# Performance work log

Measured on AMD Instinct MI355X. Metric: run time of the kernel, lower is better.

Reference implementation:

```python
import jax, jax.numpy as jnp
import numpy as np

NH = 32          # num_attention_heads
LAYER_ID = 3     # -> query_key_layer_scaling_coeff = 4.0
ROPE_BASE = 10000.0


def setup_inputs() -> dict:
    key = jax.random.key(0)
    k1, k2, k3, k4, k5 = jax.random.split(key, 5)
    S, B, H = 2048, 1, 4096
    hidden_states = jax.random.normal(k1, (S, B, H), dtype=jnp.float32)
    position_ids = jnp.broadcast_to(jnp.arange(S, dtype=jnp.int64)[None, :], (B, S))
    # causal mask: True means masked out (torch masked_fill semantics)
    mask = jnp.triu(jnp.ones((S, S), dtype=bool), k=1)[None, None, :, :]
    qkv_w = jax.random.normal(k2, (3 * H, H), dtype=jnp.float32) * 0.02
    qkv_b = jax.random.normal(k3, (3 * H,), dtype=jnp.float32) * 0.02
    dense_w = jax.random.normal(k4, (H, H), dtype=jnp.float32) * 0.02
    dense_b = jax.random.normal(k5, (H,), dtype=jnp.float32) * 0.02
    return {"hidden_states": hidden_states, "position_ids": position_ids, "mask": mask,
            "qkv_w": qkv_w, "qkv_b": qkv_b, "dense_w": dense_w, "dense_b": dense_b}


def _rotate_half(x):
    h = x.shape[-1] // 2
    return jnp.concatenate((-x[..., h:], x[..., :h]), axis=-1)


def reference(hidden_states, position_ids, mask, qkv_w, qkv_b, dense_w, dense_b):
    S, B, H = hidden_states.shape
    nh = NH
    hd = H // nh
    coeff = float(LAYER_ID + 1)

    # fused QKV projection: [S, B, 3H] -> [S, B, nh, 3*hd] -> split
    mixed = hidden_states @ qkv_w.T + qkv_b
    mixed = mixed.reshape(S, B, nh, 3 * hd)
    q, k, v = jnp.split(mixed, 3, axis=-1)  # each [S, B, nh, hd]

    # rotary embedding indexed by position_ids (transposed to [S, B])
    pos = position_ids.T  # [S, B]
    inv_freq = 1.0 / (ROPE_BASE ** (jnp.arange(0, hd, 2, dtype=jnp.float32) / hd))
    freqs = pos.astype(jnp.float32)[..., None] * inv_freq  # [S, B, hd/2]
    emb = jnp.concatenate((freqs, freqs), axis=-1)          # [S, B, hd]
    cos = jnp.cos(emb)[:, :, None, :]                       # [S, B, 1, hd]
    sin = jnp.sin(emb)[:, :, None, :]
    q = q * cos + _rotate_half(q) * sin
    k = k * cos + _rotate_half(k) * sin

    # scaled attention scores with per-layer coefficient
    q = q / (jnp.sqrt(jnp.float32(hd)) * coeff)
    scores = jnp.einsum('sbnh,tbnh->bnst', q, k)            # [B, nh, S, S]
    scores = jnp.where(mask, jnp.float32(-10000.0), scores)
    probs = jax.nn.softmax(scores.astype(jnp.float32) * coeff, axis=-1)
    probs = probs.astype(scores.dtype)

    context = jnp.einsum('bnst,tbnh->sbnh', probs, v).reshape(S, B, H)
    output = context @ dense_w.T + dense_b                  # [S, B, H]
    return output
```

## Files before the change

kernel.cpp:

```cpp
#include <hip/hip_runtime.h>
#include <hip/hip_bf16.h>
#include <cstdint>

#define SQ   2048
#define HIDD 4096
#define NH_  32
#define HD_  128

typedef __attribute__((ext_vector_type(8))) __bf16 bf16x8;
typedef __attribute__((ext_vector_type(4))) float  f32x4;

__device__ __forceinline__ unsigned short f2bf(float f) {
  union { float f; unsigned u; } v; v.f = f;
  return (unsigned short)((v.u + 0x7FFFu + ((v.u >> 16) & 1u)) >> 16);
}
__device__ __forceinline__ float bf2f(unsigned short u) {
  union { unsigned u; float f; } v; v.u = ((unsigned)u) << 16; return v.f;
}
__device__ __forceinline__ void gload16(const void* g, void* l) {
  __builtin_amdgcn_global_load_lds((const __attribute__((address_space(1))) void*)g,
                                   (__attribute__((address_space(3))) void*)l, 16, 0, 0);
}
#define BAR()   asm volatile("s_barrier" ::: "memory")
#define VMC(N)  asm volatile("s_waitcnt vmcnt(" #N ")" ::: "memory")

__global__ __launch_bounds__(256) void k_conv(const float* __restrict__ src,
                                              unsigned short* __restrict__ dst, int n4) {
  int i = blockIdx.x * blockDim.x + threadIdx.x;
  int stride = gridDim.x * blockDim.x;
  for (; i < n4; i += stride) {
    float4 f = ((const float4*)src)[i];
    ushort4 o;
    o.x = f2bf(f.x); o.y = f2bf(f.y); o.z = f2bf(f.z); o.w = f2bf(f.w);
    ((ushort4*)dst)[i] = o;
  }
}

template<int MODE>
__global__ __launch_bounds__(256, 3)
void k_gemm4(const unsigned short* __restrict__ A, const unsigned short* __restrict__ B,
             const float* __restrict__ bias, float* __restrict__ outf,
             unsigned short* __restrict__ qb, unsigned short* __restrict__ kb,
             unsigned short* __restrict__ vb, int K) {
  __shared__ __align__(16) char lds[2 * 24576];
  const int t = threadIdx.x;
  const int lane = t & 63, wc = t >> 6;
  const int lr = lane & 15, lg = lane >> 4;
  const int gx = gridDim.x;
  const int nwg = gx * gridDim.y;
  const int id = blockIdx.y * gx + blockIdx.x;
  const int cpx = nwg >> 3;
  const int swz = (id & 7) * cpx + (id >> 3);
  const int bm = swz % gx, bn = swz / gx;

  const unsigned short* src[6];
  int dst[6];
#pragma unroll
  for (int j = 0; j < 6; ++j) {
    int o = j * 4096 + t * 16;
    dst[j] = o;
    if (o < 8192) {
      int row = o >> 6, colb = o & 63;
      src[j] = A + (size_t)(bm * 128 + row) * K + ((colb ^ ((row & 3) << 4)) >> 1);
    } else {
      int o2 = o - 8192;
      int row = o2 >> 6, colb = o2 & 63;
      src[j] = B + (size_t)(bn * 256 + row) * K + ((colb ^ ((row & 3) << 4)) >> 1);
    }
  }

  f32x4 acc[8][4] = {};
  const int nk = K >> 5;
  const int swF = (lr & 3) << 4;

#pragma unroll
  for (int j = 0; j < 6; ++j) gload16(src[j], lds + dst[j]);

  int c = 0;
  for (int kt = 0; kt < nk; ++kt) {
    char* const bufc = lds + c * 24576;
    char* const bufn = lds + (c ^ 1) * 24576;
    if (kt + 1 < nk) {
      const int koff = (kt + 1) * 32;
#pragma unroll
      for (int j = 0; j < 6; ++j) gload16(src[j] + koff, bufn + dst[j]);
      VMC(6);
    } else {
      VMC(0);
    }
    BAR();

    bf16x8 bfr[4];
#pragma unroll
    for (int n = 0; n < 4; ++n) {
      int row = wc * 64 + n * 16 + lr;
      bfr[n] = *(const bf16x8*)(bufc + 8192 + row * 64 + ((lg * 16) ^ swF));
    }
    __builtin_amdgcn_s_setprio(1);
#pragma unroll
    for (int m = 0; m < 8; ++m) {
      bf16x8 a0 = *(const bf16x8*)(bufc + (m * 16 + lr) * 64 + ((lg * 16) ^ swF));
#pragma unroll
      for (int n = 0; n < 4; ++n)
        acc[m][n] = __builtin_amdgcn_mfma_f32_16x16x32_bf16(a0, bfr[n], acc[m][n], 0, 0, 0);
    }
    __builtin_amdgcn_s_setprio(0);
    BAR();
    c ^= 1;
  }

#pragma unroll
  for (int m = 0; m < 8; ++m) {
    int row0 = bm * 128 + m * 16 + lg * 4;
#pragma unroll
    for (int n = 0; n < 4; ++n) {
      int col = bn * 256 + wc * 64 + n * 16 + lr;
      float bv = bias[col];
      if (MODE == 0) {
        int h = col / 384, rem = col - h * 384;
        int sel = rem >> 7, d = rem & 127;
        unsigned short* dstp = sel == 0 ? qb : (sel == 1 ? kb : vb);
#pragma unroll
        for (int r = 0; r < 4; ++r)
          dstp[((size_t)h * SQ + row0 + r) * HD_ + d] = f2bf(acc[m][n][r] + bv);
      } else {
#pragma unroll
        for (int r = 0; r < 4; ++r)
          outf[(size_t)(row0 + r) * HIDD + col] = acc[m][n][r] + bv;
      }
    }
  }
}

template<int MODE, int BN_>
__global__ __launch_bounds__(256, 2)
void k_gemm3(const unsigned short* __restrict__ A, const unsigned short* __restrict__ B,
             const float* __restrict__ bias, float* __restrict__ outf,
             unsigned short* __restrict__ qb, unsigned short* __restrict__ kb,
             unsigned short* __restrict__ vb, int K) {
  constexpr int NS   = 4 + BN_ / 32;
  constexpr int NF   = BN_ / 64;
  constexpr int BUFB = 16384 + BN_ * 128;
  __shared__ __align__(16) char lds[2 * BUFB];
  const int t = threadIdx.x;
  const int lane = t & 63, wc = t >> 6;
  const int lr = lane & 15, lg = lane >> 4;
  const int gx = gridDim.x;
  const int nwg = gx * gridDim.y;
  const int id = blockIdx.y * gx + blockIdx.x;
  const int cpx = nwg >> 3;
  const int swz = (id & 7) * cpx + (id >> 3);
  const int bm = swz % gx, bn = swz / gx;

  const unsigned short* src[NS];
  int dst[NS];
#pragma unroll
  for (int j = 0; j < NS; ++j) {
    int o = j * 4096 + t * 16;
    dst[j] = o;
    if (o < 16384) {
      int row = o >> 7, colb = o & 127;
      src[j] = A + (size_t)(bm * 128 + row) * K + ((colb ^ ((row & 7) << 4)) >> 1);
    } else {
      int o2 = o - 16384;
      int row = o2 >> 7, colb = o2 & 127;
      src[j] = B + (size_t)(bn * BN_ + row) * K + ((colb ^ ((row & 7) << 4)) >> 1);
    }
  }

  f32x4 acc[8][NF] = {};
  const int nk = K >> 6;
  const int swA = (lr & 7) << 4;

#pragma unroll
  for (int j = 0; j < NS; ++j) gload16(src[j], lds + dst[j]);

  int c = 0;
  for (int kt = 0; kt < nk; ++kt) {
    char* const bufc = lds + c * BUFB;
    char* const bufn = lds + (c ^ 1) * BUFB;
    if (kt + 1 < nk) {
      const int koff = (kt + 1) * 64;
#pragma unroll
      for (int j = 0; j < NS; ++j) gload16(src[j] + koff, bufn + dst[j]);
      if constexpr (NS == 10) VMC(10); else VMC(8);
    } else {
      VMC(0);
    }
    BAR();

    bf16x8 bfr[NF][2];
#pragma unroll
    for (int n = 0; n < NF; ++n) {
      const char* base = bufc + 16384 + (wc * (BN_ / 4) + n * 16 + lr) * 128;
#pragma unroll
      for (int kk = 0; kk < 2; ++kk)
        bfr[n][kk] = *(const bf16x8*)(base + ((kk * 64 + lg * 16) ^ swA));
    }
    __builtin_amdgcn_s_setprio(1);
#pragma unroll
    for (int m = 0; m < 8; ++m) {
      const char* abase = bufc + (m * 16 + lr) * 128;
      bf16x8 a0 = *(const bf16x8*)(abase + ((lg * 16) ^ swA));
      bf16x8 a1 = *(const bf16x8*)(abase + ((64 + lg * 16) ^ swA));
#pragma unroll
      for (int n = 0; n < NF; ++n) {
        acc[m][n] = __builtin_amdgcn_mfma_f32_16x16x32_bf16(a0, bfr[n][0], acc[m][n], 0, 0, 0);
        acc[m][n] = __builtin_amdgcn_mfma_f32_16x16x32_bf16(a1, bfr[n][1], acc[m][n], 0, 0, 0);
      }
    }
    __builtin_amdgcn_s_setprio(0);
    BAR();
    c ^= 1;
  }

#pragma unroll
  for (int m = 0; m < 8; ++m) {
    int row0 = bm * 128 + m * 16 + lg * 4;
#pragma unroll
    for (int n = 0; n < NF; ++n) {
      int col = bn * BN_ + wc * (BN_ / 4) + n * 16 + lr;
      float bv = bias[col];
      if (MODE == 0) {
        int h = col / 384, rem = col - h * 384;
        int sel = rem >> 7, d = rem & 127;
        unsigned short* dstp = sel == 0 ? qb : (sel == 1 ? kb : vb);
#pragma unroll
        for (int r = 0; r < 4; ++r)
          dstp[((size_t)h * SQ + row0 + r) * HD_ + d] = f2bf(acc[m][n][r] + bv);
      } else {
#pragma unroll
        for (int r = 0; r < 4; ++r)
          outf[(size_t)(row0 + r) * HIDD + col] = acc[m][n][r] + bv;
      }
    }
  }
}

__global__ __launch_bounds__(256) void k_rope(unsigned short* __restrict__ q,
                                              unsigned short* __restrict__ k) {
  int idx = blockIdx.x * blockDim.x + threadIdx.x;
  int i = idx & 63;
  int s = (idx >> 6) & (SQ - 1);
  int h = idx >> 17;
  float inv = __expf(-(float)i * (9.210340371976184f / 64.0f));
  float f = (float)s * inv;
  float sn, cs;
  sincosf(f, &sn, &cs);
  size_t base = ((size_t)h * SQ + s) * HD_ + i;
  const float qs = 0.08838834764831845f;
  float q0 = bf2f(q[base]), q1 = bf2f(q[base + 64]);
  q[base]      = f2bf((q0 * cs - q1 * sn) * qs);
  q[base + 64] = f2bf((q1 * cs + q0 * sn) * qs);
  float k0 = bf2f(k[base]), k1 = bf2f(k[base + 64]);
  k[base]      = f2bf(k0 * cs - k1 * sn);
  k[base + 64] = f2bf(k1 * cs + k0 * sn);
}

__global__ __launch_bounds__(256) void k_trans(const unsigned short* __restrict__ v,
                                               unsigned short* __restrict__ vt) {
  __shared__ unsigned short tile[32][33];
  const int h = blockIdx.z;
  const int sb = blockIdx.x * 32, db = blockIdx.y * 32;
  const unsigned short* src = v + (size_t)h * SQ * HD_;
  unsigned short* dst = vt + (size_t)h * HD_ * SQ;
  for (int r = threadIdx.y; r < 32; r += 8)
    tile[r][threadIdx.x] = src[(size_t)(sb + r) * HD_ + db + threadIdx.x];
  __syncthreads();
  for (int r = threadIdx.y; r < 32; r += 8)
    dst[(size_t)(db + r) * SQ + sb + threadIdx.x] = tile[threadIdx.x][r];
}

__global__ __launch_bounds__(256)
void k_attn(const unsigned short* __restrict__ q, const unsigned short* __restrict__ k,
            const unsigned short* __restrict__ vt, unsigned short* __restrict__ ctx) {
  __shared__ __align__(16) unsigned short Ks[64 * 128];
  __shared__ __align__(16) unsigned short Vs[128 * 64];
  __shared__ __align__(16) unsigned short Ps[4][16 * 64];

  const int h = blockIdx.y;
  const int t = threadIdx.x;
  const int lane = t & 63, wv = t >> 6;
  const int lr = lane & 15, lg = lane >> 4;

  const unsigned short* Kg = k + (size_t)h * SQ * HD_;
  const unsigned short* Vg = vt + (size_t)h * HD_ * SQ;
  char* const kl = (char*)Ks;
  char* const vl = (char*)Vs;
  char* const pb = (char*)(Ps[wv]);

  for (int ph = 0; ph < 2; ++ph) {
    const int tph = (ph == 0) ? (int)blockIdx.x : 31 - (int)blockIdx.x;
    const int q0p = tph * 64;
    const int qrow = wv * 16 + lg * 4;

    const unsigned short* Q = q + ((size_t)h * SQ + q0p + wv * 16) * HD_;
    bf16x8 qf[4];
#pragma unroll
    for (int kk = 0; kk < 4; ++kk)
      qf[kk] = *(const bf16x8*)(Q + (size_t)lr * HD_ + kk * 32 + lg * 8);

    f32x4 ot[8] = {};
    float m_r[4], l_r[4];
#pragma unroll
    for (int r = 0; r < 4; ++r) { m_r[r] = -1e30f; l_r[r] = 0.f; }

    const int nkt = tph + 1;
    for (int kt = 0; kt < nkt; ++kt) {
      const int kv0 = kt * 64;
      __syncthreads();
#pragma unroll
      for (int it = 0; it < 4; ++it) {
        int o = it * 4096 + t * 16;
        int krow = o >> 8, kcb = o & 255;
        int kscb = kcb ^ ((krow & 7) << 4);
        gload16(Kg + (size_t)(kv0 + krow) * HD_ + (kscb >> 1), kl + o);
        int vrow = o >> 7, vcb = o & 127;
        int vscb = vcb ^ ((vrow & 7) << 4);
        gload16(Vg + (size_t)vrow * SQ + kv0 + (vscb >> 1), vl + o);
      }
      __syncthreads();

      f32x4 sc[4] = {};
#pragma unroll
      for (int ct = 0; ct < 4; ++ct) {
        int row = ct * 16 + lr;
        const char* kbase = kl + row * 256;
#pragma unroll
        for (int kk = 0; kk < 4; ++kk) {
          bf16x8 kf = *(const bf16x8*)(kbase + ((kk * 64 + lg * 16) ^ ((row & 7) << 4)));
          sc[ct] = __builtin_amdgcn_mfma_f32_16x16x32_bf16(qf[kk], kf, sc[ct], 0, 0, 0);
        }
      }

      if (kt == tph) {
#pragma unroll
        for (int ct = 0; ct < 4; ++ct) {
          int col = ct * 16 + lr;
#pragma unroll
          for (int r = 0; r < 4; ++r)
            if (col > qrow + r) sc[ct][r] = -1e30f;
        }
      }

      float tmax[4];
#pragma unroll
      for (int r = 0; r < 4; ++r)
        tmax[r] = fmaxf(fmaxf(sc[0][r], sc[1][r]), fmaxf(sc[2][r], sc[3][r]));
#pragma unroll
      for (int off = 1; off < 16; off <<= 1)
#pragma unroll
        for (int r = 0; r < 4; ++r) tmax[r] = fmaxf(tmax[r], __shfl_xor(tmax[r], off, 64));

      float scf[4];
#pragma unroll
      for (int r = 0; r < 4; ++r) {
        float mn = fmaxf(m_r[r], tmax[r]);
        scf[r] = __expf(m_r[r] - mn);
        m_r[r] = mn;
      }
      float pr[4][4], rsum[4];
#pragma unroll
      for (int r = 0; r < 4; ++r) rsum[r] = 0.f;
#pragma unroll
      for (int ct = 0; ct < 4; ++ct)
#pragma unroll
        for (int r = 0; r < 4; ++r) {
          pr[ct][r] = __expf(sc[ct][r] - m_r[r]);
          rsum[r] += pr[ct][r];
        }
#pragma unroll
      for (int off = 1; off < 16; off <<= 1)
#pragma unroll
        for (int r = 0; r < 4; ++r) rsum[r] += __shfl_xor(rsum[r], off, 64);
#pragma unroll
      for (int r = 0; r < 4; ++r) l_r[r] = l_r[r] * scf[r] + rsum[r];

#pragma unroll
      for (int dt = 0; dt < 8; ++dt)
#pragma unroll
        for (int r = 0; r < 4; ++r) ot[dt][r] *= scf[r];

#pragma unroll
      for (int ct = 0; ct < 4; ++ct)
#pragma unroll
        for (int r = 0; r < 4; ++r) {
          int row = lg * 4 + r;
          int byte = row * 128 + ((ct * 32 + lr * 2) ^ ((row & 7) << 4));
          *(unsigned short*)(pb + byte) = f2bf(pr[ct][r]);
        }
      bf16x8 pa[2];
#pragma unroll
      for (int k2 = 0; k2 < 2; ++k2)
        pa[k2] = *(const bf16x8*)(pb + lr * 128 + ((k2 * 64 + lg * 16) ^ ((lr & 7) << 4)));

#pragma unroll
      for (int dt = 0; dt < 8; ++dt) {
        int row = dt * 16 + lr;
        const char* vbase = vl + row * 128;
        bf16x8 vf0 = *(const bf16x8*)(vbase + ((lg * 16) ^ ((row & 7) << 4)));
        bf16x8 vf1 = *(const bf16x8*)(vbase + ((64 + lg * 16) ^ ((row & 7) << 4)));
        ot[dt] = __builtin_amdgcn_mfma_f32_16x16x32_bf16(pa[0], vf0, ot[dt], 0, 0, 0);
        ot[dt] = __builtin_amdgcn_mfma_f32_16x16x32_bf16(pa[1], vf1, ot[dt], 0, 0, 0);
      }
    }

    float inv[4];
#pragma unroll
    for (int r = 0; r < 4; ++r) inv[r] = 1.0f / l_r[r];
#pragma unroll
    for (int dt = 0; dt < 8; ++dt)
#pragma unroll
      for (int r = 0; r < 4; ++r)
        ctx[(size_t)(q0p + wv * 16 + lg * 4 + r) * HIDD + h * HD_ + dt * 16 + lr] =
            f2bf(ot[dt][r] * inv[r]);
  }
}

extern "C" void kernel_launch(void* const* d_in, const int* in_sizes, int n_in,
                              void* d_out, int out_size, void* d_ws, size_t ws_size,
                              hipStream_t stream) {
  const float* hidden  = (const float*)d_in[0];
  const float* qkv_w   = (const float*)d_in[3];
  const float* qkv_b   = (const float*)d_in[4];
  const float* dense_w = (const float*)d_in[5];
  const float* dense_b = (const float*)d_in[6];
  float* out = (float*)d_out;

  char* ws = (char*)d_ws;
  unsigned short* wbuf = (unsigned short*)ws;
  unsigned short* hidb = (unsigned short*)(ws + 100663296);
  unsigned short* vtb  = hidb;
  unsigned short* qb   = (unsigned short*)(ws + 117440512);
  unsigned short* kb   = (unsigned short*)(ws + 134217728);
  unsigned short* vb   = (unsigned short*)(ws + 150994944);
  unsigned short* ctx  = (unsigned short*)(ws + 167772160);
  if (ws_size < 184549376ull) return;

  k_conv<<<2048, 256, 0, stream>>>(hidden, hidb, 8388608 / 4);
  k_conv<<<4096, 256, 0, stream>>>(qkv_w, wbuf, 50331648 / 4);
  k_gemm4<0><<<dim3(16, 48), 256, 0, stream>>>(hidb, wbuf, qkv_b, nullptr, qb, kb, vb, 4096);
  k_rope<<<16384, 256, 0, stream>>>(qb, kb);
  k_trans<<<dim3(64, 4, 32), dim3(32, 8), 0, stream>>>(vb, vtb);
  k_attn<<<dim3(16, 32), 256, 0, stream>>>(qb, kb, vtb, ctx);
  k_conv<<<2048, 256, 0, stream>>>(dense_w, wbuf, 16777216 / 4);
  k_gemm3<1, 128><<<dim3(16, 32), 256, 0, stream>>>(ctx, wbuf, dense_b, out, nullptr, nullptr, nullptr, 4096);
}
```

Before: 479.9 us.

## Replace QKV GEMM with 256x256-tile 8-wave kernel and interleaved load phases

The QKV projection GEMM moves from a 128x256 tile with 4 waves and a K-step of 32 to a 256x256 tile with 8 waves (2x4 wave grid) and a K-step of 64, using 128 KB of double-buffered LDS. Each K iteration is split into four MFMA quadrants, and the next tile's global-to-LDS loads are issued in pieces between them, so memory traffic overlaps compute. The aim is more data reuse per byte loaded and better latency hiding. In exchange, only one workgroup fits per CU because of the LDS use, the grid drops to 384 blocks, and there are more barriers per iteration.

```diff
diff --git a/kernel.cpp b/kernel.cpp
--- a/kernel.cpp
+++ b/kernel.cpp
@@ -23,6 +23,7 @@
 }
 #define BAR()   asm volatile("s_barrier" ::: "memory")
 #define VMC(N)  asm volatile("s_waitcnt vmcnt(" #N ")" ::: "memory")
+#define MFMA_(a, b, c) __builtin_amdgcn_mfma_f32_16x16x32_bf16(a, b, c, 0, 0, 0)
 
 __global__ __launch_bounds__(256) void k_conv(const float* __restrict__ src,
                                               unsigned short* __restrict__ dst, int n4) {
@@ -37,15 +38,16 @@
 }
 
 template<int MODE>
-__global__ __launch_bounds__(256, 3)
-void k_gemm4(const unsigned short* __restrict__ A, const unsigned short* __restrict__ B,
+__global__ __launch_bounds__(512, 2)
+void k_gemm8(const unsigned short* __restrict__ A, const unsigned short* __restrict__ B,
              const float* __restrict__ bias, float* __restrict__ outf,
              unsigned short* __restrict__ qb, unsigned short* __restrict__ kb,
              unsigned short* __restrict__ vb, int K) {
-  __shared__ __align__(16) char lds[2 * 24576];
+  __shared__ __align__(16) char lds[131072];
   const int t = threadIdx.x;
-  const int lane = t & 63, wc = t >> 6;
+  const int lane = t & 63, wid = t >> 6;
   const int lr = lane & 15, lg = lane >> 4;
+  const int wr = wid >> 2, wcq = wid & 3;
   const int gx = gridDim.x;
   const int nwg = gx * gridDim.y;
   const int id = blockIdx.y * gx + blockIdx.x;
@@ -53,68 +55,123 @@
   const int swz = (id & 7) * cpx + (id >> 3);
   const int bm = swz % gx, bn = swz / gx;
 
-  const unsigned short* src[6];
-  int dst[6];
-#pragma unroll
-  for (int j = 0; j < 6; ++j) {
-    int o = j * 4096 + t * 16;
-    dst[j] = o;
-    if (o < 8192) {
-      int row = o >> 6, colb = o & 63;
-      src[j] = A + (size_t)(bm * 128 + row) * K + ((colb ^ ((row & 3) << 4)) >> 1);
-    } else {
-      int o2 = o - 8192;
-      int row = o2 >> 6, colb = o2 & 63;
-      src[j] = B + (size_t)(bn * 256 + row) * K + ((colb ^ ((row & 3) << 4)) >> 1);
-    }
-  }
+  const int o = t * 16;
+  const int srow = o >> 7;
+  const int sc2 = ((o & 127) ^ ((srow & 7) << 4)) >> 1;
+  const int srowK = srow * K;
+
+  auto stA = [&](int g, int koff, char* buf) {
+    gload16(A + (size_t)(bm * 256 + g * 64) * K + (srowK + sc2 + koff), buf + g * 8192 + o);
+  };
+  auto stB = [&](int g, int koff, char* buf) {
+    gload16(B + (size_t)(bn * 256 + g * 64) * K + (srowK + sc2 + koff), buf + 32768 + g * 8192 + o);
+  };
 
   f32x4 acc[8][4] = {};
-  const int nk = K >> 5;
-  const int swF = (lr & 3) << 4;
-
-#pragma unroll
-  for (int j = 0; j < 6; ++j) gload16(src[j], lds + dst[j]);
-
-  int c = 0;
+  const int nk = K >> 6;
+  const int swA = (lr & 7) << 4;
+  const int rowb = lr * 128;
+  const int fo0 = (lg * 16) ^ swA;
+  const int fo1 = (64 + lg * 16) ^ swA;
+
+  stA(0, 0, lds); stA(1, 0, lds);
+  stB(0, 0, lds); stB(1, 0, lds);
+  stA(2, 0, lds); stA(3, 0, lds);
+  stB(2, 0, lds); stB(3, 0, lds);
+  VMC(4); BAR();
+
   for (int kt = 0; kt < nk; ++kt) {
-    char* const bufc = lds + c * 24576;
-    char* const bufn = lds + (c ^ 1) * 24576;
-    if (kt + 1 < nk) {
-      const int koff = (kt + 1) * 32;
-#pragma unroll
-      for (int j = 0; j < 6; ++j) gload16(src[j] + koff, bufn + dst[j]);
-      VMC(6);
-    } else {
-      VMC(0);
-    }
-    BAR();
-
-    bf16x8 bfr[4];
+    char* const bufc = lds + (kt & 1) * 65536;
+    char* const bufn = lds + ((kt & 1) ^ 1) * 65536;
+    const bool pre = (kt + 1 < nk);
+    const int koff = (kt + 1) * 64;
+    const char* pa = bufc + rowb;
+    const char* pb = bufc + 32768 + rowb;
+    bf16x8 a0[4][2], a1[4][2], b0r[2][2], b1r[2][2];
+
+#pragma unroll
+    for (int f = 0; f < 4; ++f) {
+      const char* base = pa + (f * 2 + wr) * 2048;
+      a0[f][0] = *(const bf16x8*)(base + fo0);
+      a0[f][1] = *(const bf16x8*)(base + fo1);
+    }
+#pragma unroll
+    for (int n = 0; n < 2; ++n) {
+      const char* base = pb + (n * 4 + wcq) * 2048;
+      b0r[n][0] = *(const bf16x8*)(base + fo0);
+      b0r[n][1] = *(const bf16x8*)(base + fo1);
+    }
+    if (pre) { stA(0, koff, bufn); stA(1, koff, bufn); VMC(4); } else { VMC(2); }
+    BAR();
+    __builtin_amdgcn_s_setprio(1);
+#pragma unroll
+    for (int f = 0; f < 4; ++f)
+#pragma unroll
+      for (int n = 0; n < 2; ++n) {
+        acc[f][n] = MFMA_(a0[f][0], b0r[n][0], acc[f][n]);
+        acc[f][n] = MFMA_(a0[f][1], b0r[n][1], acc[f][n]);
+      }
+    __builtin_amdgcn_s_setprio(0);
+    BAR();
+
+#pragma unroll
+    for (int f = 0; f < 4; ++f) {
+      const char* base = pa + ((f + 4) * 2 + wr) * 2048;
+      a1[f][0] = *(const bf16x8*)(base + fo0);
+      a1[f][1] = *(const bf16x8*)(base + fo1);
+    }
+    if (pre) { stB(0, koff, bufn); stB(1, koff, bufn); VMC(4); } else { VMC(0); }
+    BAR();
+    __builtin_amdgcn_s_setprio(1);
+#pragma unroll
+    for (int f = 0; f < 4; ++f)
+#pragma unroll
+      for (int n = 0; n < 2; ++n) {
+        acc[f + 4][n] = MFMA_(a1[f][0], b0r[n][0], acc[f + 4][n]);
+        acc[f + 4][n] = MFMA_(a1[f][1], b0r[n][1], acc[f + 4][n]);
+      }
+    __builtin_amdgcn_s_setprio(0);
+    BAR();
+
+#pragma unroll
+    for (int n = 0; n < 2; ++n) {
+      const char* base = pb + ((n + 2) * 4 + wcq) * 2048;
+      b1r[n][0] = *(const bf16x8*)(base + fo0);
+      b1r[n][1] = *(const bf16x8*)(base + fo1);
+    }
+    if (pre) { stA(2, koff, bufn); stA(3, koff, bufn); }
+    BAR();
+    __builtin_amdgcn_s_setprio(1);
+#pragma unroll
+    for (int f = 0; f < 4; ++f)
+#pragma unroll
+      for (int n = 0; n < 2; ++n) {
+        acc[f + 4][n + 2] = MFMA_(a1[f][0], b1r[n][0], acc[f + 4][n + 2]);
+        acc[f + 4][n + 2] = MFMA_(a1[f][1], b1r[n][1], acc[f + 4][n + 2]);
+      }
+    __builtin_amdgcn_s_setprio(0);
+    BAR();
+
+    if (pre) { stB(2, koff, bufn); stB(3, koff, bufn); VMC(4); }
+    BAR();
+    __builtin_amdgcn_s_setprio(1);
+#pragma unroll
+    for (int f = 0; f < 4; ++f)
+#pragma unroll
+      for (int n = 0; n < 2; ++n) {
+        acc[f][n + 2] = MFMA_(a0[f][0], b1r[n][0], acc[f][n + 2]);
+        acc[f][n + 2] = MFMA_(a0[f][1], b1r[n][1], acc[f][n + 2]);
+      }
+    __builtin_amdgcn_s_setprio(0);
+    BAR();
+  }
+
+#pragma unroll
+  for (int f = 0; f < 8; ++f) {
+    int row0 = bm * 256 + (f * 2 + wr) * 16 + lg * 4;
 #pragma unroll
     for (int n = 0; n < 4; ++n) {
-      int row = wc * 64 + n * 16 + lr;
-      bfr[n] = *(const bf16x8*)(bufc + 8192 + row * 64 + ((lg * 16) ^ swF));
-    }
-    __builtin_amdgcn_s_setprio(1);
-#pragma unroll
-    for (int m = 0; m < 8; ++m) {
-      bf16x8 a0 = *(const bf16x8*)(bufc + (m * 16 + lr) * 64 + ((lg * 16) ^ swF));
-#pragma unroll
-      for (int n = 0; n < 4; ++n)
-        acc[m][n] = __builtin_amdgcn_mfma_f32_16x16x32_bf16(a0, bfr[n], acc[m][n], 0, 0, 0);
-    }
-    __builtin_amdgcn_s_setprio(0);
-    BAR();
-    c ^= 1;
-  }
-
-#pragma unroll
-  for (int m = 0; m < 8; ++m) {
-    int row0 = bm * 128 + m * 16 + lg * 4;
-#pragma unroll
-    for (int n = 0; n < 4; ++n) {
-      int col = bn * 256 + wc * 64 + n * 16 + lr;
+      int col = bn * 256 + (n * 4 + wcq) * 16 + lr;
       float bv = bias[col];
       if (MODE == 0) {
         int h = col / 384, rem = col - h * 384;
@@ -122,11 +179,11 @@
         unsigned short* dstp = sel == 0 ? qb : (sel == 1 ? kb : vb);
 #pragma unroll
         for (int r = 0; r < 4; ++r)
-          dstp[((size_t)h * SQ + row0 + r) * HD_ + d] = f2bf(acc[m][n][r] + bv);
+          dstp[((size_t)h * SQ + row0 + r) * HD_ + d] = f2bf(acc[f][n][r] + bv);
       } else {
 #pragma unroll
         for (int r = 0; r < 4; ++r)
-          outf[(size_t)(row0 + r) * HIDD + col] = acc[m][n][r] + bv;
+          outf[(size_t)(row0 + r) * HIDD + col] = acc[f][n][r] + bv;
       }
     }
   }
@@ -205,8 +262,8 @@
       bf16x8 a1 = *(const bf16x8*)(abase + ((64 + lg * 16) ^ swA));
 #pragma unroll
       for (int n = 0; n < NF; ++n) {
-        acc[m][n] = __builtin_amdgcn_mfma_f32_16x16x32_bf16(a0, bfr[n][0], acc[m][n], 0, 0, 0);
-        acc[m][n] = __builtin_amdgcn_mfma_f32_16x16x32_bf16(a1, bfr[n][1], acc[m][n], 0, 0, 0);
+        acc[m][n] = MFMA_(a0, bfr[n][0], acc[m][n]);
+        acc[m][n] = MFMA_(a1, bfr[n][1], acc[m][n]);
       }
     }
     __builtin_amdgcn_s_setprio(0);
@@ -329,7 +386,7 @@
 #pragma unroll
         for (int kk = 0; kk < 4; ++kk) {
           bf16x8 kf = *(const bf16x8*)(kbase + ((kk * 64 + lg * 16) ^ ((row & 7) << 4)));
-          sc[ct] = __builtin_amdgcn_mfma_f32_16x16x32_bf16(qf[kk], kf, sc[ct], 0, 0, 0);
+          sc[ct] = MFMA_(qf[kk], kf, sc[ct]);
         }
       }
 
@@ -400,8 +457,8 @@
         const char* vbase = vl + row * 128;
         bf16x8 vf0 = *(const bf16x8*)(vbase + ((lg * 16) ^ ((row & 7) << 4)));
         bf16x8 vf1 = *(const bf16x8*)(vbase + ((64 + lg * 16) ^ ((row & 7) << 4)));
-        ot[dt] = __builtin_amdgcn_mfma_f32_16x16x32_bf16(pa[0], vf0, ot[dt], 0, 0, 0);
-        ot[dt] = __builtin_amdgcn_mfma_f32_16x16x32_bf16(pa[1], vf1, ot[dt], 0, 0, 0);
+        ot[dt] = MFMA_(pa[0], vf0, ot[dt]);
+        ot[dt] = MFMA_(pa[1], vf1, ot[dt]);
       }
     }
 
@@ -439,7 +496,7 @@
 
   k_conv<<<2048, 256, 0, stream>>>(hidden, hidb, 8388608 / 4);
   k_conv<<<4096, 256, 0, stream>>>(qkv_w, wbuf, 50331648 / 4);
-  k_gemm4<0><<<dim3(16, 48), 256, 0, stream>>>(hidb, wbuf, qkv_b, nullptr, qb, kb, vb, 4096);
+  k_gemm8<0><<<dim3(8, 48), 512, 0, stream>>>(hidb, wbuf, qkv_b, nullptr, qb, kb, vb, 4096);
   k_rope<<<16384, 256, 0, stream>>>(qb, kb);
   k_trans<<<dim3(64, 4, 32), dim3(32, 8), 0, stream>>>(vb, vtb);
   k_attn<<<dim3(16, 32), 256, 0, stream>>>(qb, kb, vtb, ctx);
```

Result: slower. 497.0 us (+3.6%).
